# Kernel optimization log

Measured on AMD Instinct MI355X. Metric: run time of the kernel, lower is better.

Reference implementation:

```python
import jax, jax.numpy as jnp
import numpy as np

NH = 12      # config.n_head
LEVEL = 2    # config.level -> Lmin = 4


def setup_inputs() -> dict:
    key = jax.random.key(0)
    ks = jax.random.split(key, 10)
    B, T, C = 1, 2048, 768
    hs = C // NH
    s = 0.02
    return {
        'x':   jax.random.normal(ks[0], (B, T, C), jnp.float32),
        'Wq':  jax.random.normal(ks[1], (C, C), jnp.float32) * s,
        'Wk':  jax.random.normal(ks[2], (C, C), jnp.float32) * s,
        'Wv':  jax.random.normal(ks[3], (C, C), jnp.float32) * s,
        'Wks': jax.random.normal(ks[4], (hs * hs, hs), jnp.float32) * s,
        'bks': jax.random.normal(ks[5], (hs,), jnp.float32) * s,
        'Wvs': jax.random.normal(ks[6], (hs * hs, hs), jnp.float32) * s,
        'bvs': jax.random.normal(ks[7], (hs,), jnp.float32) * s,
        'Wc':  jax.random.normal(ks[8], (C, C), jnp.float32) * s,
        'bc':  jax.random.normal(ks[9], (C,), jnp.float32) * s,
    }


def reference(x, Wq, Wk, Wv, Wks, bks, Wvs, bvs, Wc, bc):
    B, T, C = x.shape
    hs = C // NH
    Lmin = 2 ** LEVEL
    levelmax = int(np.log2(T))          # T is a power of two -> no ragged tails per level
    scale = hs ** -0.5

    # fla LinearAttention preprocess: bias-free projections + elu feature map (phi = elu+1)
    q = (jax.nn.elu(x @ Wq) + 1.0).reshape(B, T, NH, hs)
    k = (jax.nn.elu(x @ Wk) + 1.0).reshape(B, T, NH, hs)
    v = (x @ Wv).reshape(B, T, NH, hs)

    # per-position linear-attn state increments phi(k) v^T  [B,T,H,hs,hs]
    kv = jnp.einsum('bthi,bthj->bthij', k, v).reshape(B, T, NH, hs * hs)

    # tail features: running state within each block of Lmin (fused_recurrent final states
    # over the ragged per-position tail segments [t - t%Lmin, t])
    tail_feat = jnp.cumsum(kv.reshape(B, T // Lmin, Lmin, NH, hs * hs), axis=2)
    tail_feat = tail_feat.reshape(B, T, NH, hs * hs)

    # hierarchical set features: dyadic block sums at levels LEVEL..levelmax
    cur = kv.reshape(B, T // Lmin, Lmin, NH, hs * hs).sum(axis=2)
    feats, ends = [], []
    for l in range(LEVEL, levelmax + 1):
        n = T // (2 ** l)
        feats.append(cur)
        ends.append(np.arange(1, n + 1) * (2 ** l))   # exclusive end index of each set
        if n >= 2:
            cur = cur.reshape(B, n // 2, 2, NH, hs * hs).sum(axis=2)
    set_feat = jnp.concatenate(feats, axis=1)          # [B, S, H, hs*hs], S = 1023
    ends = np.concatenate(ends)                        # [S]
    mask = ends[None, :] <= (np.arange(T) + 1)[:, None]  # [T, S] causal set mask

    # k_mapping / v_mapping: Linear(hs^2 -> hs)
    K = set_feat @ Wks + bks        # [B,S,H,hs]
    V = set_feat @ Wvs + bvs
    K_tail = tail_feat @ Wks + bks  # [B,T,H,hs]
    V_tail = tail_feat @ Wvs + bvs

    logits = jnp.einsum('bthd,bshd->bhts', q, K) * scale      # [B,H,T,S]
    logits = jnp.where(mask[None, None], logits, jnp.float32(-1e30))
    tail_logit = jnp.einsum('bthd,bthd->bht', q, K_tail) * scale  # [B,H,T]
    att = jax.nn.softmax(jnp.concatenate([logits, tail_logit[..., None]], axis=-1), axis=-1)

    out = jnp.einsum('bhts,bshd->bhtd', att[..., :-1], V)
    out = out + att[..., -1:] * V_tail.transpose(0, 2, 1, 3)  # [B,H,T,hs]
    out = out.transpose(0, 2, 1, 3).reshape(B, T, C)
    return out @ Wc + bc
```

## Files before the change

kernel.cpp:

```cpp
#include <hip/hip_runtime.h>
#include <cstdint>

#define NHEAD 12
#define TLEN 2048
#define CDIM 768
#define NSETS 1023

typedef __attribute__((ext_vector_type(8))) _Float16 half8;
typedef __attribute__((ext_vector_type(2))) __fp16 fp16x2;
typedef __attribute__((ext_vector_type(8))) short short8;
typedef __attribute__((ext_vector_type(4))) float f32x4;

__device__ __forceinline__ float elu1(float x) { return x > 0.f ? x + 1.f : __expf(x); }

__device__ __forceinline__ unsigned pack2_bf16_trunc(float a, float b) {
    unsigned ua = __float_as_uint(a), ub = __float_as_uint(b);
    return __builtin_amdgcn_perm(ub, ua, 0x07060302);
}
__device__ __forceinline__ unsigned pack2_bf16_rne(float a, float b) {
    unsigned ua = __float_as_uint(a), ub = __float_as_uint(b);
    ua = ua + 0x7fff + ((ua >> 16) & 1);
    ub = ub + 0x7fff + ((ub >> 16) & 1);
    return (ub & 0xffff0000u) | (ua >> 16);
}
__device__ __forceinline__ short8 mk_short8(const unsigned* u) {
    union { unsigned w[4]; short8 s; } x;
    x.w[0] = u[0]; x.w[1] = u[1]; x.w[2] = u[2]; x.w[3] = u[3];
    return x.s;
}
__device__ __forceinline__ void split8_bf16(const float* f, short8& hi, short8& lo) {
    unsigned hp[4], lp[4];
    #pragma unroll
    for (int p = 0; p < 4; ++p) {
        float a = f[2 * p], b = f[2 * p + 1];
        unsigned ua = __float_as_uint(a), ub = __float_as_uint(b);
        hp[p] = __builtin_amdgcn_perm(ub, ua, 0x07060302);
        float ra = a - __uint_as_float(ua & 0xffff0000u);
        float rb = b - __uint_as_float(ub & 0xffff0000u);
        lp[p] = pack2_bf16_trunc(ra, rb);
    }
    hi = mk_short8(hp); lo = mk_short8(lp);
}
__device__ __forceinline__ void split8_f16(const float* f, half8& hi, half8& lo) {
    union { fp16x2 h2[4]; half8 h8; } uh, ul;
    #pragma unroll
    for (int jp = 0; jp < 4; ++jp) {
        float a = f[2 * jp], b = f[2 * jp + 1];
        fp16x2 hh = __builtin_amdgcn_cvt_pkrtz(a, b);
        uh.h2[jp] = hh;
        ul.h2[jp] = __builtin_amdgcn_cvt_pkrtz(a - (float)hh[0], b - (float)hh[1]);
    }
    hi = uh.h8; lo = ul.h8;
}

__global__ __launch_bounds__(256) void prep_all(
    const float* __restrict__ Wq, const float* __restrict__ Wk,
    const float* __restrict__ Wv, const float* __restrict__ Wc4,
    const float* __restrict__ Wks, const float* __restrict__ Wvs,
    const float* __restrict__ x,
    _Float16* __restrict__ blobQKV, _Float16* __restrict__ blobC,
    _Float16* __restrict__ Wblob,
    _Float16* __restrict__ xhi, _Float16* __restrict__ xlo)
{
    const int g = blockIdx.x;
    const int tid = threadIdx.x;
    if (g < 9216) {
        const int sel = g / 2304;
        const float* W = sel == 0 ? Wq : (sel == 1 ? Wk : (sel == 2 ? Wv : Wc4));
        _Float16* blob = (sel < 3) ? (blobQKV + (size_t)sel * 589824) : blobC;
        const int idx = (g % 2304) * 256 + tid;
        const int k = idx / 768, n = idx % 768;
        const int i = k >> 5, kl = k & 31;
        const int quad = kl >> 3, j = kl & 7;
        const int nsg = n >> 4, lane15 = n & 15;
        const int lane = quad * 16 + lane15;
        blob[((size_t)(i * 48 + nsg) * 64 + lane) * 8 + j] = (_Float16)W[idx];
    } else if (g < 9216 + 2048) {
        const int idx = (g - 9216) * 256 + tid;
        const int kk = idx >> 7, n = idx & 127;
        float f = (n < 64) ? Wks[(size_t)kk * 64 + n] : Wvs[(size_t)kk * 64 + (n - 64)];
        const int i = kk >> 6, kl = kk & 63;
        const int ks = kl >> 5, quad = (kl >> 3) & 3, j = kl & 7;
        const int nsg = n >> 4, lane15 = n & 15;
        const int lane = quad * 16 + lane15;
        const size_t off = ((size_t)(((i * 2 + ks) * 8 + nsg)) * 64 + lane) * 8 + j;
        Wblob[off] = (_Float16)f;
    } else {
        const int p = (g - 11264) * 256 + tid;
        const int lane = p & 63, frag = p >> 6;
        const int m16 = frag / 24, k32 = frag - m16 * 24;
        const int row = m16 * 16 + (lane & 15);
        const int col = k32 * 32 + (lane >> 4) * 8;
        float f[8];
        *(float4*)&f[0] = *(const float4*)&x[(size_t)row * CDIM + col];
        *(float4*)&f[4] = *(const float4*)&x[(size_t)row * CDIM + col + 4];
        half8 h, l;
        split8_f16(f, h, l);
        *(half8*)&xhi[(size_t)p * 8] = h;
        *(half8*)&xlo[(size_t)p * 8] = l;
    }
}

template<int QKV>
__global__ __launch_bounds__(256, 3) void gemm_frag(
    const _Float16* __restrict__ Ahi, const _Float16* __restrict__ Alo,
    const _Float16* __restrict__ Bblobs, const float* __restrict__ bias,
    float* __restrict__ outq, unsigned* __restrict__ kdup,
    _Float16* __restrict__ v16)
{
    const int nbx = QKV ? 18 : 6;
    const int cpx = QKV ? 72 : 24;
    int bid = blockIdx.x;
    bid = (bid & 7) * cpx + (bid >> 3);
    const int by  = bid / nbx;
    const int bxg = bid % nbx;
    const int which = QKV ? bxg / 6 : 0;
    const int bxm   = QKV ? bxg % 6 : bxg;
    const half8* __restrict__ Bc = (const half8*)(Bblobs + (size_t)which * 589824);

    const int tid = threadIdx.x;
    const int wave = tid >> 6, lane = tid & 63;
    const int lane15 = lane & 15, quad = lane >> 4;
    const int m16b = by * 4;
    const int nsg0 = bxm * 8 + wave * 2;

    const half8* __restrict__ Ah = (const half8*)Ahi;
    const half8* __restrict__ Al = (const half8*)Alo;

    f32x4 acc[4][2];
    #pragma unroll
    for (int ms = 0; ms < 4; ++ms) {
        acc[ms][0] = (f32x4){0.f, 0.f, 0.f, 0.f};
        acc[ms][1] = (f32x4){0.f, 0.f, 0.f, 0.f};
    }

    const size_t aBase = ((size_t)m16b * 24) * 64 + lane;
    const size_t bBase = (size_t)nsg0 * 64 + lane;

    half8 bb[2], ah[4], al[4];
    bb[0] = Bc[bBase];
    bb[1] = Bc[bBase + 64];
    #pragma unroll
    for (int ms = 0; ms < 4; ++ms) {
        ah[ms] = Ah[aBase + (size_t)ms * (24 * 64)];
        al[ms] = Al[aBase + (size_t)ms * (24 * 64)];
    }

    for (int k32 = 0; k32 < 24; ++k32) {
        half8 bbn[2], ahn[4], aln[4];
        const bool more = (k32 + 1) < 24;
        if (more) {
            const size_t bo = bBase + (size_t)(k32 + 1) * (48 * 64);
            bbn[0] = Bc[bo]; bbn[1] = Bc[bo + 64];
            #pragma unroll
            for (int ms = 0; ms < 4; ++ms) {
                const size_t ao = aBase + (size_t)(k32 + 1) * 64 + (size_t)ms * (24 * 64);
                ahn[ms] = Ah[ao]; aln[ms] = Al[ao];
            }
        }
        #pragma unroll
        for (int ms = 0; ms < 4; ++ms) {
            acc[ms][0] = __builtin_amdgcn_mfma_f32_16x16x32_f16(ah[ms], bb[0], acc[ms][0], 0, 0, 0);
            acc[ms][1] = __builtin_amdgcn_mfma_f32_16x16x32_f16(ah[ms], bb[1], acc[ms][1], 0, 0, 0);
            acc[ms][0] = __builtin_amdgcn_mfma_f32_16x16x32_f16(al[ms], bb[0], acc[ms][0], 0, 0, 0);
            acc[ms][1] = __builtin_amdgcn_mfma_f32_16x16x32_f16(al[ms], bb[1], acc[ms][1], 0, 0, 0);
        }
        if (more) {
            bb[0] = bbn[0]; bb[1] = bbn[1];
            #pragma unroll
            for (int ms = 0; ms < 4; ++ms) { ah[ms] = ahn[ms]; al[ms] = aln[ms]; }
        }
    }

    #pragma unroll
    for (int ms = 0; ms < 4; ++ms)
        #pragma unroll
        for (int nb = 0; nb < 2; ++nb) {
            const int coln = (nsg0 + nb) * 16 + lane15;
            #pragma unroll
            for (int r = 0; r < 4; ++r) {
                const int row = m16b * 16 + ms * 16 + quad * 4 + r;
                float vv = acc[ms][nb][r];
                if (!QKV) {
                    outq[(size_t)row * CDIM + coln] = vv + bias[coln];
                } else if (which == 0) {
                    outq[(size_t)row * CDIM + coln] = elu1(vv);
                } else if (which == 1) {
                    float e = elu1(vv);
                    union { fp16x2 h; unsigned u; } cc;
                    cc.h = __builtin_amdgcn_cvt_pkrtz(e, e);
                    kdup[(size_t)row * CDIM + coln] = cc.u;
                } else {
                    union { fp16x2 h; _Float16 f2[2]; } cc;
                    cc.h = __builtin_amdgcn_cvt_pkrtz(vv, vv);
                    v16[(size_t)row * CDIM + coln] = cc.f2[0];
                }
            }
        }
}

__global__ __launch_bounds__(256, 2) void map_f16(
    const unsigned* __restrict__ kdup, const _Float16* __restrict__ v16,
    const _Float16* __restrict__ Wblob,
    float* __restrict__ kkv, float* __restrict__ vvv)
{
    __shared__ unsigned kU[64][65];

    const int tid = threadIdx.x;
    const int p0 = blockIdx.x * 64;
    const int wave = tid >> 6, lane = tid & 63;
    const int lane15 = lane & 15, quad = lane >> 4;

    {
        const int row = tid >> 2, cb = (tid & 3) * 16;
        const unsigned* src = &kdup[(size_t)(p0 + row) * 64 + cb];
        uint4 a0 = *(const uint4*)(src + 0);
        uint4 a1 = *(const uint4*)(src + 4);
        uint4 a2 = *(const uint4*)(src + 8);
        uint4 a3 = *(const uint4*)(src + 12);
        *(uint4*)&kU[row][cb + 0]  = a0;
        *(uint4*)&kU[row][cb + 4]  = a1;
        *(uint4*)&kU[row][cb + 8]  = a2;
        *(uint4*)&kU[row][cb + 12] = a3;
    }

    half8 vrh[4][2];
    #pragma unroll
    for (int mh = 0; mh < 4; ++mh) {
        const size_t pbase = (size_t)(p0 + mh * 16 + lane15) * 64;
        #pragma unroll
        for (int ks = 0; ks < 2; ++ks)
            vrh[mh][ks] = *(const half8*)&v16[pbase + ks * 32 + quad * 8];
    }
    __syncthreads();

    const half8* __restrict__ Wc = (const half8*)Wblob;

    f32x4 acc[4][2];
    #pragma unroll
    for (int mh = 0; mh < 4; ++mh)
        #pragma unroll
        for (int nsl = 0; nsl < 2; ++nsl)
            acc[mh][nsl] = (f32x4){0.f, 0.f, 0.f, 0.f};

    half8 b0[2], b1[2], b2[2], b3[2];
    unsigned ka0[4], ka1[4], ka2[4], ka3[4];

    auto loadB = [&](half8* b, int s) {
        b[0] = Wc[(size_t)(s * 8 + 2 * wave) * 64 + lane];
        b[1] = Wc[(size_t)(s * 8 + 2 * wave + 1) * 64 + lane];
    };
    auto loadK = [&](unsigned* ka, int s) {
        const int i = s >> 1;
        #pragma unroll
        for (int mh = 0; mh < 4; ++mh) ka[mh] = kU[mh * 16 + lane15][i];
    };
    auto compute = [&](const half8* b, const unsigned* ka, int s) {
        const int ks = s & 1;
        #pragma unroll
        for (int mh = 0; mh < 4; ++mh) {
            union { unsigned u; fp16x2 h; } ku; ku.u = ka[mh];
            union { fp16x2 h2[4]; half8 h8; } va, ra;
            va.h8 = vrh[mh][ks];
            #pragma unroll
            for (int jp = 0; jp < 4; ++jp) ra.h2[jp] = ku.h * va.h2[jp];
            acc[mh][0] = __builtin_amdgcn_mfma_f32_16x16x32_f16(ra.h8, b[0], acc[mh][0], 0, 0, 0);
            acc[mh][1] = __builtin_amdgcn_mfma_f32_16x16x32_f16(ra.h8, b[1], acc[mh][1], 0, 0, 0);
        }
    };

    loadB(b0, 0); loadB(b1, 1); loadB(b2, 2); loadB(b3, 3);
    loadK(ka0, 0); loadK(ka1, 1); loadK(ka2, 2); loadK(ka3, 3);
    for (int s = 0; s < 128; s += 4) {
        const bool more = (s + 4) < 128;
        compute(b0, ka0, s);
        compute(b1, ka1, s + 1);
        if (more) { loadB(b0, s + 4); loadK(ka0, s + 4); loadB(b1, s + 5); loadK(ka1, s + 5); }
        compute(b2, ka2, s + 2);
        compute(b3, ka3, s + 3);
        if (more) { loadB(b2, s + 6); loadK(ka2, s + 6); loadB(b3, s + 7); loadK(ka3, s + 7); }
    }

    #pragma unroll
    for (int mh = 0; mh < 4; ++mh)
        #pragma unroll
        for (int nsl = 0; nsl < 2; ++nsl) {
            int n128 = (2 * wave + nsl) * 16 + lane15;
            float* dst = (n128 < 64) ? kkv : vvv;
            int col = n128 & 63;
            #pragma unroll
            for (int r = 0; r < 4; ++r) {
                int p = p0 + mh * 16 + quad * 4 + r;
                dst[(size_t)p * 64 + col] = acc[mh][nsl][r];
            }
        }
}

__global__ __launch_bounds__(256) void set_lower(
    const float* __restrict__ kkv, const float* __restrict__ vvv,
    const float* __restrict__ bks, const float* __restrict__ bvs,
    float* __restrict__ Kset, float* __restrict__ Vset,
    float* __restrict__ scrK, float* __restrict__ scrV,
    float* __restrict__ Kt, float* __restrict__ Vt)
{
    __shared__ float curK[63][64];
    __shared__ float curV[63][64];
    const int tid = threadIdx.x;
    const int col = tid & 63, grp = tid >> 6;
    const int h = blockIdx.x % NHEAD;
    const int c = blockIdx.x / NHEAD;
    const int t0 = c * 128;
    const float bk = bks[col], bv = bvs[col];

    for (int j = grp; j < 32; j += 4) {
        const size_t rbase = (size_t)(t0 + j * 4) * CDIM + h * 64 + col;
        const float* pk = kkv + rbase;
        const float* pv = vvv + rbase;
        float* ptK = Kt + rbase;
        float* ptV = Vt + rbase;
        float sk = bk, sv = bv;
        #pragma unroll
        for (int u = 0; u < 4; ++u) {
            sk += pk[(size_t)u * CDIM];
            sv += pv[(size_t)u * CDIM];
            ptK[(size_t)u * CDIM] = sk;
            ptV[(size_t)u * CDIM] = sv;
        }
        curK[j][col] = sk - bk; curV[j][col] = sv - bv;
        size_t o = ((size_t)(c * 32 + j) * NHEAD + h) * 64 + col;
        Kset[o] = sk; Vset[o] = sv;
    }
    __syncthreads();

    const int LBASE[6] = {0, 32, 48, 56, 60, 62};
    const int GBASE[6] = {0, 512, 768, 896, 960, 992};
    #pragma unroll
    for (int li = 1; li < 6; ++li) {
        const int ns = 32 >> li;
        for (int j = grp; j < ns; j += 4) {
            float sk = curK[LBASE[li - 1] + 2 * j][col] + curK[LBASE[li - 1] + 2 * j + 1][col];
            float sv = curV[LBASE[li - 1] + 2 * j][col] + curV[LBASE[li - 1] + 2 * j + 1][col];
            curK[LBASE[li] + j][col] = sk; curV[LBASE[li] + j][col] = sv;
            size_t o = ((size_t)(GBASE[li] + c * ns + j) * NHEAD + h) * 64 + col;
            Kset[o] = sk + bk; Vset[o] = sv + bv;
        }
        __syncthreads();
    }

    if (grp == 0) {
        scrK[((size_t)h * 16 + c) * 64 + col] = curK[62][col];
        scrV[((size_t)h * 16 + c) * 64 + col] = curV[62][col];
    }
}

__global__ __launch_bounds__(256) void set_upper(
    const float* __restrict__ scrK, const float* __restrict__ scrV,
    const float* __restrict__ bks, const float* __restrict__ bvs,
    float* __restrict__ Kset, float* __restrict__ Vset)
{
    __shared__ float cK[15][64], cV[15][64];
    const int h = blockIdx.x;
    const int tid = threadIdx.x, col = tid & 63, grp = tid >> 6;
    const float bk = bks[col], bv = bvs[col];

    for (int j = grp; j < 8; j += 4) {
        float sk = scrK[((size_t)h * 16 + 2 * j) * 64 + col] + scrK[((size_t)h * 16 + 2 * j + 1) * 64 + col];
        float sv = scrV[((size_t)h * 16 + 2 * j) * 64 + col] + scrV[((size_t)h * 16 + 2 * j + 1) * 64 + col];
        cK[j][col] = sk; cV[j][col] = sv;
        size_t o = ((size_t)(1008 + j) * NHEAD + h) * 64 + col;
        Kset[o] = sk + bk; Vset[o] = sv + bv;
    }
    __syncthreads();
    const int LB[4] = {0, 8, 12, 14};
    const int GB[4] = {1008, 1016, 1020, 1022};
    #pragma unroll
    for (int li = 1; li < 4; ++li) {
        const int ns = 8 >> li;
        for (int j = grp; j < ns; j += 4) {
            float sk = cK[LB[li - 1] + 2 * j][col] + cK[LB[li - 1] + 2 * j + 1][col];
            float sv = cV[LB[li - 1] + 2 * j][col] + cV[LB[li - 1] + 2 * j + 1][col];
            cK[LB[li] + j][col] = sk; cV[LB[li] + j][col] = sv;
            size_t o = ((size_t)(GB[li] + j) * NHEAD + h) * 64 + col;
            Kset[o] = sk + bk; Vset[o] = sv + bv;
        }
        __syncthreads();
    }
}

__global__ __launch_bounds__(256, 3) void attn_mfma(
    const float* __restrict__ qbuf, const float* __restrict__ Kset,
    const float* __restrict__ Vset, const float* __restrict__ Ktail,
    const float* __restrict__ Vtail,
    _Float16* __restrict__ atthi, _Float16* __restrict__ attlo)
{
    __shared__ unsigned ssAll[1024];
    __shared__ float sS[2][32][68];
    __shared__ unsigned sP[2][32][40];
    __shared__ unsigned vP[2][64][40];
    __shared__ float arowS[2][32];
    __shared__ float alS[32], ptS[32];

    const int tid = threadIdx.x;
    const int b   = 63 - (blockIdx.x / NHEAD);
    const int h   = blockIdx.x % NHEAD;
    const int T0  = b * 32;
    const int wave = tid >> 6, lane = tid & 63;
    const int lane15 = lane & 15, quad = lane >> 4;

    const int Tend = T0 + 32;
    const int LOFF[10] = {0, 512, 768, 896, 960, 992, 1008, 1016, 1020, 1022};
    int pfx[10], Vtot = 0;
    #pragma unroll
    for (int li = 0; li < 10; ++li) { pfx[li] = Vtot; Vtot += Tend >> (li + 2); }
    const int ntiles = (Vtot + 63) >> 6;

    for (int j = tid; j < 1024; j += 256) {
        unsigned pk = (4095u << 16);
        if (j < Vtot) {
            int li = 0;
            #pragma unroll
            for (int u = 1; u < 10; ++u) if (j >= pfx[u]) li = u;
            int idx = j - pfx[li];
            pk = (unsigned)(LOFF[li] + idx) | ((unsigned)((idx + 1) << (li + 2)) << 16);
        }
        ssAll[j] = pk;
    }

    short8 Qhi[2][2], Qlo[2][2];
    #pragma unroll
    for (int ms = 0; ms < 2; ++ms)
        #pragma unroll
        for (int kt = 0; kt < 2; ++kt) {
            const float* qp = qbuf + ((size_t)(T0 + ms * 16 + lane15) * NHEAD + h) * 64 + kt * 32 + quad * 8;
            float f[8];
            *(float4*)&f[0] = *(const float4*)qp;
            *(float4*)&f[4] = *(const float4*)(qp + 4);
            split8_bf16(f, Qhi[ms][kt], Qlo[ms][kt]);
        }

    __syncthreads();

    const int row = tid >> 3, part = tid & 7;
    float mreg = -1e30f, lreg = 0.f;

    f32x4 oacc[2];
    oacc[0] = (f32x4){0.f, 0.f, 0.f, 0.f};
    oacc[1] = (f32x4){0.f, 0.f, 0.f, 0.f};

    float4 Vr[4];
    float4 Kr[4];
    const int sp = tid >> 3, dd = (tid & 7) * 8;
    auto prefV = [&](int tile) {
        int sa = (int)(ssAll[tile * 64 + 2 * sp] & 0xffffu);
        int sb = (int)(ssAll[tile * 64 + 2 * sp + 1] & 0xffffu);
        const float* pa = Vset + ((size_t)sa * NHEAD + h) * 64 + dd;
        const float* pb = Vset + ((size_t)sb * NHEAD + h) * 64 + dd;
        Vr[0] = *(const float4*)pa; Vr[1] = *(const float4*)(pa + 4);
        Vr[2] = *(const float4*)pb; Vr[3] = *(const float4*)(pb + 4);
    };
    auto prefK = [&](int tile) {
        int sK = (int)(ssAll[tile * 64 + wave * 16 + lane15] & 0xffffu);
        const float* kp = Kset + ((size_t)sK * NHEAD + h) * 64 + quad * 8;
        Kr[0] = *(const float4*)kp;        Kr[1] = *(const float4*)(kp + 4);
        Kr[2] = *(const float4*)(kp + 32); Kr[3] = *(const float4*)(kp + 36);
    };
    prefV(0); prefK(0);

    for (int tile = 0; tile < ntiles; ++tile) {
        const int c = tile & 1;

        {
            const float* va = (const float*)&Vr[0];
            const float* vb = (const float*)&Vr[2];
            #pragma unroll
            for (int i = 0; i < 8; ++i)
                vP[c][dd + i][sp] = pack2_bf16_rne(va[i], vb[i]);
        }

        short8 Khi[2], Klo[2];
        {
            float f[8];
            *(float4*)&f[0] = Kr[0]; *(float4*)&f[4] = Kr[1];
            split8_bf16(f, Khi[0], Klo[0]);
            *(float4*)&f[0] = Kr[2]; *(float4*)&f[4] = Kr[3];
            split8_bf16(f, Khi[1], Klo[1]);
        }

        f32x4 lacc[2];
        lacc[0] = (f32x4){0.f, 0.f, 0.f, 0.f};
        lacc[1] = (f32x4){0.f, 0.f, 0.f, 0.f};
        #pragma unroll
        for (int kt = 0; kt < 2; ++kt)
            #pragma unroll
            for (int ms = 0; ms < 2; ++ms) {
                lacc[ms] = __builtin_amdgcn_mfma_f32_16x16x32_bf16(Qhi[ms][kt], Khi[kt], lacc[ms], 0, 0, 0);
                lacc[ms] = __builtin_amdgcn_mfma_f32_16x16x32_bf16(Qlo[ms][kt], Khi[kt], lacc[ms], 0, 0, 0);
                lacc[ms] = __builtin_amdgcn_mfma_f32_16x16x32_bf16(Qhi[ms][kt], Klo[kt], lacc[ms], 0, 0, 0);
            }

        {
            const int sendv = (int)(ssAll[tile * 64 + wave * 16 + lane15] >> 16);
            #pragma unroll
            for (int ms = 0; ms < 2; ++ms)
                #pragma unroll
                for (int r = 0; r < 4; ++r) {
                    int qrow = ms * 16 + quad * 4 + r;
                    bool ok = (T0 + qrow + 1) >= sendv;
                    sS[c][qrow][wave * 16 + lane15] = ok ? lacc[ms][r] * 0.125f : -1e30f;
                }
        }

        if (tile + 1 < ntiles) { prefV(tile + 1); prefK(tile + 1); }

        __syncthreads();

        {
            float4 a = *(float4*)&sS[c][row][part * 8];
            float4 c4 = *(float4*)&sS[c][row][part * 8 + 4];
            float mx = fmaxf(fmaxf(fmaxf(a.x, a.y), fmaxf(a.z, a.w)),
                             fmaxf(fmaxf(c4.x, c4.y), fmaxf(c4.z, c4.w)));
            mx = fmaxf(mx, __shfl_xor(mx, 1));
            mx = fmaxf(mx, __shfl_xor(mx, 2));
            mx = fmaxf(mx, __shfl_xor(mx, 4));
            float mnew = fmaxf(mreg, mx);
            float al = __expf(mreg - mnew);
            mreg = mnew;
            a.x = a.x > -1e29f ? __expf(a.x - mnew) : 0.f;
            a.y = a.y > -1e29f ? __expf(a.y - mnew) : 0.f;
            a.z = a.z > -1e29f ? __expf(a.z - mnew) : 0.f;
            a.w = a.w > -1e29f ? __expf(a.w - mnew) : 0.f;
            c4.x = c4.x > -1e29f ? __expf(c4.x - mnew) : 0.f;
            c4.y = c4.y > -1e29f ? __expf(c4.y - mnew) : 0.f;
            c4.z = c4.z > -1e29f ? __expf(c4.z - mnew) : 0.f;
            c4.w = c4.w > -1e29f ? __expf(c4.w - mnew) : 0.f;
            float sm = (a.x + a.y + a.z + a.w) + (c4.x + c4.y + c4.z + c4.w);
            sm += __shfl_xor(sm, 1);
            sm += __shfl_xor(sm, 2);
            sm += __shfl_xor(sm, 4);
            lreg = al * lreg + sm;
            unsigned w0 = pack2_bf16_rne(a.x, a.y);
            unsigned w1 = pack2_bf16_rne(a.z, a.w);
            unsigned w2 = pack2_bf16_rne(c4.x, c4.y);
            unsigned w3 = pack2_bf16_rne(c4.z, c4.w);
            *(uint4*)&sP[c][row][part * 4] = make_uint4(w0, w1, w2, w3);
            if (part == 0) arowS[c][row] = al;
        }

        __syncthreads();

        #pragma unroll
        for (int ms = 0; ms < 2; ++ms)
            #pragma unroll
            for (int r = 0; r < 4; ++r)
                oacc[ms][r] *= arowS[c][ms * 16 + quad * 4 + r];

        #pragma unroll
        for (int kt = 0; kt < 2; ++kt) {
            short8 Vf = *(short8*)&vP[c][wave * 16 + lane15][kt * 16 + quad * 4];
            #pragma unroll
            for (int ms = 0; ms < 2; ++ms) {
                short8 Pf = *(short8*)&sP[c][ms * 16 + lane15][kt * 16 + quad * 4];
                oacc[ms] = __builtin_amdgcn_mfma_f32_16x16x32_bf16(Pf, Vf, oacc[ms], 0, 0, 0);
            }
        }
    }

    {
        const float* qr = qbuf  + ((size_t)(T0 + row) * NHEAD + h) * 64 + part * 8;
        const float* kr = Ktail + ((size_t)(T0 + row) * NHEAD + h) * 64 + part * 8;
        float4 qa = *(const float4*)qr, qb = *(const float4*)(qr + 4);
        float4 ka = *(const float4*)kr, kb = *(const float4*)(kr + 4);
        float dp = qa.x * ka.x + qa.y * ka.y + qa.z * ka.z + qa.w * ka.w
                 + qb.x * kb.x + qb.y * kb.y + qb.z * kb.z + qb.w * kb.w;
        dp += __shfl_xor(dp, 1);
        dp += __shfl_xor(dp, 2);
        dp += __shfl_xor(dp, 4);
        float tl = dp * 0.125f;
        float mf = fmaxf(mreg, tl);
        float al = __expf(mreg - mf);
        float pt = __expf(tl - mf);
        float lf = al * lreg + pt;
        float inv = 1.f / lf;
        if (part == 0) { alS[row] = al * inv; ptS[row] = pt * inv; }
    }
    __syncthreads();

    #pragma unroll
    for (int ms = 0; ms < 2; ++ms)
        #pragma unroll
        for (int r = 0; r < 4; ++r) {
            int qrow = ms * 16 + quad * 4 + r;
            int col = wave * 16 + lane15;
            size_t base = ((size_t)(T0 + qrow) * NHEAD + h) * 64 + col;
            sS[0][qrow][col] = oacc[ms][r] * alS[qrow] + ptS[qrow] * Vtail[base];
        }
    __syncthreads();

    {
        const int kt = wave >> 1, msf = wave & 1;
        float f[8];
        *(float4*)&f[0] = *(const float4*)&sS[0][msf * 16 + lane15][kt * 32 + quad * 8];
        *(float4*)&f[4] = *(const float4*)&sS[0][msf * 16 + lane15][kt * 32 + quad * 8 + 4];
        half8 hh, ll;
        split8_f16(f, hh, ll);
        const size_t frag = (size_t)(b * 2 + msf) * 24 + (2 * h + kt);
        *(half8*)&atthi[(frag * 64 + lane) * 8] = hh;
        *(half8*)&attlo[(frag * 64 + lane) * 8] = ll;
    }
}

extern "C" void kernel_launch(void* const* d_in, const int* in_sizes, int n_in,
                              void* d_out, int out_size, void* d_ws, size_t ws_size,
                              hipStream_t stream)
{
    const float* x   = (const float*)d_in[0];
    const float* Wq  = (const float*)d_in[1];
    const float* Wk  = (const float*)d_in[2];
    const float* Wv  = (const float*)d_in[3];
    const float* Wks = (const float*)d_in[4];
    const float* bks = (const float*)d_in[5];
    const float* Wvs = (const float*)d_in[6];
    const float* bvs = (const float*)d_in[7];
    const float* Wc  = (const float*)d_in[8];
    const float* bc  = (const float*)d_in[9];
    float* out = (float*)d_out;

    float* ws = (float*)d_ws;
    const size_t TC = (size_t)TLEN * CDIM;
    float* q      = ws;
    float* k      = q + TC;
    float* v      = k + TC;
    float* kkv    = v + TC;
    float* vvv    = kkv + TC;
    float* Kt     = vvv + TC;
    float* Vt     = Kt + TC;
    float* Kset   = Vt + TC;
    float* Vset   = Kset + (size_t)NSETS * CDIM;
    float* attout = Vset + (size_t)NSETS * CDIM;
    _Float16* WblobMap = (_Float16*)attout;
    _Float16* blobQKV  = (_Float16*)(attout + 262144);
    float* scrK = attout + 1146880;
    float* scrV = scrK + 12 * 16 * 64;
    _Float16* blobC = (_Float16*)(attout + 1171456);
    _Float16* xhi = (_Float16*)kkv;
    _Float16* xlo = xhi + TC;
    unsigned*  kdup = (unsigned*)k;
    _Float16*  v16  = (_Float16*)v;
    _Float16* atthi = (_Float16*)vvv;
    _Float16* attlo = atthi + TC;

    prep_all<<<9216 + 2048 + 768, 256, 0, stream>>>(
        Wq, Wk, Wv, Wc, Wks, Wvs, x, blobQKV, blobC, WblobMap, xhi, xlo);

    gemm_frag<1><<<576, 256, 0, stream>>>(xhi, xlo, blobQKV, nullptr, q, kdup, v16);

    map_f16<<<(TLEN * NHEAD) / 64, 256, 0, stream>>>(kdup, v16, WblobMap, kkv, vvv);

    set_lower<<<16 * NHEAD, 256, 0, stream>>>(kkv, vvv, bks, bvs, Kset, Vset, scrK, scrV, Kt, Vt);
    set_upper<<<NHEAD, 256, 0, stream>>>(scrK, scrV, bks, bvs, Kset, Vset);

    attn_mfma<<<(TLEN / 32) * NHEAD, 256, 0, stream>>>(q, Kset, Vset, Kt, Vt, atthi, attlo);

    gemm_frag<0><<<192, 256, 0, stream>>>(atthi, attlo, blobC, bc, out, nullptr, nullptr);
}
```

Baseline: 204.4 us.

## Store set K/V pre-split as bf16 hi/lo in producers; use exp2 softmax

The set-reduction kernels now write K as bf16 hi/lo halves and V as rounded bf16, so the attention kernel loads half-width data and skips the per-tile split and pack conversions. This cuts global gather traffic for K/V in the attention inner loop and moves conversion work out of it. The softmax scale is also folded with log2(e) so exp2f replaces __expf. The cost is slightly more store work in the set kernels and a changed workspace layout.

```diff
diff --git a/kernel.cpp b/kernel.cpp
--- a/kernel.cpp
+++ b/kernel.cpp
@@ -9,7 +9,10 @@
 typedef __attribute__((ext_vector_type(8))) _Float16 half8;
 typedef __attribute__((ext_vector_type(2))) __fp16 fp16x2;
 typedef __attribute__((ext_vector_type(8))) short short8;
+typedef __attribute__((ext_vector_type(8))) unsigned short u16x8;
 typedef __attribute__((ext_vector_type(4))) float f32x4;
+
+#define SOFTMAX_SCL 0.18033688011112042f
 
 __device__ __forceinline__ float elu1(float x) { return x > 0.f ? x + 1.f : __expf(x); }
 
@@ -23,10 +26,26 @@
     ub = ub + 0x7fff + ((ub >> 16) & 1);
     return (ub & 0xffff0000u) | (ua >> 16);
 }
+__device__ __forceinline__ unsigned short bf16_hi_trunc(float a) {
+    return (unsigned short)(__float_as_uint(a) >> 16);
+}
+__device__ __forceinline__ unsigned short bf16_lo_trunc(float a) {
+    unsigned ua = __float_as_uint(a);
+    float r = a - __uint_as_float(ua & 0xffff0000u);
+    return (unsigned short)(__float_as_uint(r) >> 16);
+}
+__device__ __forceinline__ unsigned short bf16_rne(float a) {
+    unsigned ua = __float_as_uint(a);
+    ua = ua + 0x7fff + ((ua >> 16) & 1);
+    return (unsigned short)(ua >> 16);
+}
 __device__ __forceinline__ short8 mk_short8(const unsigned* u) {
     union { unsigned w[4]; short8 s; } x;
     x.w[0] = u[0]; x.w[1] = u[1]; x.w[2] = u[2]; x.w[3] = u[3];
     return x.s;
+}
+__device__ __forceinline__ short8 as_s8(u16x8 v) {
+    union { u16x8 u; short8 s; } x; x.u = v; return x.s;
 }
 __device__ __forceinline__ void split8_bf16(const float* f, short8& hi, short8& lo) {
     unsigned hp[4], lp[4];
@@ -299,7 +318,8 @@
 __global__ __launch_bounds__(256) void set_lower(
     const float* __restrict__ kkv, const float* __restrict__ vvv,
     const float* __restrict__ bks, const float* __restrict__ bvs,
-    float* __restrict__ Kset, float* __restrict__ Vset,
+    unsigned short* __restrict__ KsetH, unsigned short* __restrict__ KsetL,
+    unsigned short* __restrict__ VsetB,
     float* __restrict__ scrK, float* __restrict__ scrV,
     float* __restrict__ Kt, float* __restrict__ Vt)
 {
@@ -328,7 +348,8 @@
         }
         curK[j][col] = sk - bk; curV[j][col] = sv - bv;
         size_t o = ((size_t)(c * 32 + j) * NHEAD + h) * 64 + col;
-        Kset[o] = sk; Vset[o] = sv;
+        KsetH[o] = bf16_hi_trunc(sk); KsetL[o] = bf16_lo_trunc(sk);
+        VsetB[o] = bf16_rne(sv);
     }
     __syncthreads();
 
@@ -342,7 +363,9 @@
             float sv = curV[LBASE[li - 1] + 2 * j][col] + curV[LBASE[li - 1] + 2 * j + 1][col];
             curK[LBASE[li] + j][col] = sk; curV[LBASE[li] + j][col] = sv;
             size_t o = ((size_t)(GBASE[li] + c * ns + j) * NHEAD + h) * 64 + col;
-            Kset[o] = sk + bk; Vset[o] = sv + bv;
+            float kv_ = sk + bk, vv_ = sv + bv;
+            KsetH[o] = bf16_hi_trunc(kv_); KsetL[o] = bf16_lo_trunc(kv_);
+            VsetB[o] = bf16_rne(vv_);
         }
         __syncthreads();
     }
@@ -356,7 +379,8 @@
 __global__ __launch_bounds__(256) void set_upper(
     const float* __restrict__ scrK, const float* __restrict__ scrV,
     const float* __restrict__ bks, const float* __restrict__ bvs,
-    float* __restrict__ Kset, float* __restrict__ Vset)
+    unsigned short* __restrict__ KsetH, unsigned short* __restrict__ KsetL,
+    unsigned short* __restrict__ VsetB)
 {
     __shared__ float cK[15][64], cV[15][64];
     const int h = blockIdx.x;
@@ -368,7 +392,9 @@
         float sv = scrV[((size_t)h * 16 + 2 * j) * 64 + col] + scrV[((size_t)h * 16 + 2 * j + 1) * 64 + col];
         cK[j][col] = sk; cV[j][col] = sv;
         size_t o = ((size_t)(1008 + j) * NHEAD + h) * 64 + col;
-        Kset[o] = sk + bk; Vset[o] = sv + bv;
+        float kv_ = sk + bk, vv_ = sv + bv;
+        KsetH[o] = bf16_hi_trunc(kv_); KsetL[o] = bf16_lo_trunc(kv_);
+        VsetB[o] = bf16_rne(vv_);
     }
     __syncthreads();
     const int LB[4] = {0, 8, 12, 14};
@@ -381,16 +407,19 @@
             float sv = cV[LB[li - 1] + 2 * j][col] + cV[LB[li - 1] + 2 * j + 1][col];
             cK[LB[li] + j][col] = sk; cV[LB[li] + j][col] = sv;
             size_t o = ((size_t)(GB[li] + j) * NHEAD + h) * 64 + col;
-            Kset[o] = sk + bk; Vset[o] = sv + bv;
+            float kv_ = sk + bk, vv_ = sv + bv;
+            KsetH[o] = bf16_hi_trunc(kv_); KsetL[o] = bf16_lo_trunc(kv_);
+            VsetB[o] = bf16_rne(vv_);
         }
         __syncthreads();
     }
 }
 
 __global__ __launch_bounds__(256, 3) void attn_mfma(
-    const float* __restrict__ qbuf, const float* __restrict__ Kset,
-    const float* __restrict__ Vset, const float* __restrict__ Ktail,
-    const float* __restrict__ Vtail,
+    const float* __restrict__ qbuf,
+    const unsigned short* __restrict__ KsetH, const unsigned short* __restrict__ KsetL,
+    const unsigned short* __restrict__ VsetB,
+    const float* __restrict__ Ktail, const float* __restrict__ Vtail,
     _Float16* __restrict__ atthi, _Float16* __restrict__ attlo)
 {
     __shared__ unsigned ssAll[1024];
@@ -447,44 +476,34 @@
     oacc[0] = (f32x4){0.f, 0.f, 0.f, 0.f};
     oacc[1] = (f32x4){0.f, 0.f, 0.f, 0.f};
 
-    float4 Vr[4];
-    float4 Kr[4];
+    u16x8 Va, Vb;
+    u16x8 KH[2], KL[2];
     const int sp = tid >> 3, dd = (tid & 7) * 8;
     auto prefV = [&](int tile) {
         int sa = (int)(ssAll[tile * 64 + 2 * sp] & 0xffffu);
         int sb = (int)(ssAll[tile * 64 + 2 * sp + 1] & 0xffffu);
-        const float* pa = Vset + ((size_t)sa * NHEAD + h) * 64 + dd;
-        const float* pb = Vset + ((size_t)sb * NHEAD + h) * 64 + dd;
-        Vr[0] = *(const float4*)pa; Vr[1] = *(const float4*)(pa + 4);
-        Vr[2] = *(const float4*)pb; Vr[3] = *(const float4*)(pb + 4);
+        Va = *(const u16x8*)(VsetB + ((size_t)sa * NHEAD + h) * 64 + dd);
+        Vb = *(const u16x8*)(VsetB + ((size_t)sb * NHEAD + h) * 64 + dd);
     };
     auto prefK = [&](int tile) {
         int sK = (int)(ssAll[tile * 64 + wave * 16 + lane15] & 0xffffu);
-        const float* kp = Kset + ((size_t)sK * NHEAD + h) * 64 + quad * 8;
-        Kr[0] = *(const float4*)kp;        Kr[1] = *(const float4*)(kp + 4);
-        Kr[2] = *(const float4*)(kp + 32); Kr[3] = *(const float4*)(kp + 36);
+        const size_t ko = ((size_t)sK * NHEAD + h) * 64 + quad * 8;
+        KH[0] = *(const u16x8*)(KsetH + ko);
+        KH[1] = *(const u16x8*)(KsetH + ko + 32);
+        KL[0] = *(const u16x8*)(KsetL + ko);
+        KL[1] = *(const u16x8*)(KsetL + ko + 32);
     };
     prefV(0); prefK(0);
 
     for (int tile = 0; tile < ntiles; ++tile) {
         const int c = tile & 1;
 
-        {
-            const float* va = (const float*)&Vr[0];
-            const float* vb = (const float*)&Vr[2];
-            #pragma unroll
-            for (int i = 0; i < 8; ++i)
-                vP[c][dd + i][sp] = pack2_bf16_rne(va[i], vb[i]);
-        }
-
-        short8 Khi[2], Klo[2];
-        {
-            float f[8];
-            *(float4*)&f[0] = Kr[0]; *(float4*)&f[4] = Kr[1];
-            split8_bf16(f, Khi[0], Klo[0]);
-            *(float4*)&f[0] = Kr[2]; *(float4*)&f[4] = Kr[3];
-            split8_bf16(f, Khi[1], Klo[1]);
-        }
+        #pragma unroll
+        for (int i = 0; i < 8; ++i)
+            vP[c][dd + i][sp] = (unsigned)Va[i] | ((unsigned)Vb[i] << 16);
+
+        short8 Khi[2] = { as_s8(KH[0]), as_s8(KH[1]) };
+        short8 Klo[2] = { as_s8(KL[0]), as_s8(KL[1]) };
 
         f32x4 lacc[2];
         lacc[0] = (f32x4){0.f, 0.f, 0.f, 0.f};
@@ -506,7 +525,7 @@
                 for (int r = 0; r < 4; ++r) {
                     int qrow = ms * 16 + quad * 4 + r;
                     bool ok = (T0 + qrow + 1) >= sendv;
-                    sS[c][qrow][wave * 16 + lane15] = ok ? lacc[ms][r] * 0.125f : -1e30f;
+                    sS[c][qrow][wave * 16 + lane15] = ok ? lacc[ms][r] * SOFTMAX_SCL : -1e30f;
                 }
         }
 
@@ -523,16 +542,16 @@
             mx = fmaxf(mx, __shfl_xor(mx, 2));
             mx = fmaxf(mx, __shfl_xor(mx, 4));
             float mnew = fmaxf(mreg, mx);
-            float al = __expf(mreg - mnew);
+            float al = exp2f(mreg - mnew);
             mreg = mnew;
-            a.x = a.x > -1e29f ? __expf(a.x - mnew) : 0.f;
-            a.y = a.y > -1e29f ? __expf(a.y - mnew) : 0.f;
-            a.z = a.z > -1e29f ? __expf(a.z - mnew) : 0.f;
-            a.w = a.w > -1e29f ? __expf(a.w - mnew) : 0.f;
-            c4.x = c4.x > -1e29f ? __expf(c4.x - mnew) : 0.f;
-            c4.y = c4.y > -1e29f ? __expf(c4.y - mnew) : 0.f;
-            c4.z = c4.z > -1e29f ? __expf(c4.z - mnew) : 0.f;
-            c4.w = c4.w > -1e29f ? __expf(c4.w - mnew) : 0.f;
+            a.x = a.x > -1e29f ? exp2f(a.x - mnew) : 0.f;
+            a.y = a.y > -1e29f ? exp2f(a.y - mnew) : 0.f;
+            a.z = a.z > -1e29f ? exp2f(a.z - mnew) : 0.f;
+            a.w = a.w > -1e29f ? exp2f(a.w - mnew) : 0.f;
+            c4.x = c4.x > -1e29f ? exp2f(c4.x - mnew) : 0.f;
+            c4.y = c4.y > -1e29f ? exp2f(c4.y - mnew) : 0.f;
+            c4.z = c4.z > -1e29f ? exp2f(c4.z - mnew) : 0.f;
+            c4.w = c4.w > -1e29f ? exp2f(c4.w - mnew) : 0.f;
             float sm = (a.x + a.y + a.z + a.w) + (c4.x + c4.y + c4.z + c4.w);
             sm += __shfl_xor(sm, 1);
             sm += __shfl_xor(sm, 2);
@@ -575,10 +594,10 @@
         dp += __shfl_xor(dp, 1);
         dp += __shfl_xor(dp, 2);
         dp += __shfl_xor(dp, 4);
-        float tl = dp * 0.125f;
+        float tl = dp * SOFTMAX_SCL;
         float mf = fmaxf(mreg, tl);
-        float al = __expf(mreg - mf);
-        float pt = __expf(tl - mf);
+        float al = exp2f(mreg - mf);
+        float pt = exp2f(tl - mf);
         float lf = al * lreg + pt;
         float inv = 1.f / lf;
         if (part == 0) { alS[row] = al * inv; ptS[row] = pt * inv; }
@@ -634,14 +653,15 @@
     float* vvv    = kkv + TC;
     float* Kt     = vvv + TC;
     float* Vt     = Kt + TC;
-    float* Kset   = Vt + TC;
-    float* Vset   = Kset + (size_t)NSETS * CDIM;
-    float* attout = Vset + (size_t)NSETS * CDIM;
-    _Float16* WblobMap = (_Float16*)attout;
-    _Float16* blobQKV  = (_Float16*)(attout + 262144);
-    float* scrK = attout + 1146880;
+    float* base   = Vt + TC;
+    _Float16* WblobMap = (_Float16*)base;
+    _Float16* blobQKV  = (_Float16*)(base + 262144);
+    float* scrK = base + 1146880;
     float* scrV = scrK + 12 * 16 * 64;
-    _Float16* blobC = (_Float16*)(attout + 1171456);
+    _Float16* blobC = (_Float16*)(base + 1171456);
+    unsigned short* KsetH = (unsigned short*)(base + 1466368);
+    unsigned short* KsetL = KsetH + 786432;
+    unsigned short* VsetB = KsetL + 786432;
     _Float16* xhi = (_Float16*)kkv;
     _Float16* xlo = xhi + TC;
     unsigned*  kdup = (unsigned*)k;
@@ -656,10 +676,10 @@
 
     map_f16<<<(TLEN * NHEAD) / 64, 256, 0, stream>>>(kdup, v16, WblobMap, kkv, vvv);
 
-    set_lower<<<16 * NHEAD, 256, 0, stream>>>(kkv, vvv, bks, bvs, Kset, Vset, scrK, scrV, Kt, Vt);
-    set_upper<<<NHEAD, 256, 0, stream>>>(scrK, scrV, bks, bvs, Kset, Vset);
-
-    attn_mfma<<<(TLEN / 32) * NHEAD, 256, 0, stream>>>(q, Kset, Vset, Kt, Vt, atthi, attlo);
+    set_lower<<<16 * NHEAD, 256, 0, stream>>>(kkv, vvv, bks, bvs, KsetH, KsetL, VsetB, scrK, scrV, Kt, Vt);
+    set_upper<<<NHEAD, 256, 0, stream>>>(scrK, scrV, bks, bvs, KsetH, KsetL, VsetB);
+
+    attn_mfma<<<(TLEN / 32) * NHEAD, 256, 0, stream>>>(q, KsetH, KsetL, VsetB, Kt, Vt, atthi, attlo);
 
     gemm_frag<0><<<192, 256, 0, stream>>>(atthi, attlo, blobC, bc, out, nullptr, nullptr);
 }
```

Measured after the change: 200.5 us. No clear change (-1.9%).
